# Optimization experiments

Measured on AMD Instinct MI355X. Metric: run time of the kernel, lower is better.

## Reference

```python
import jax, jax.numpy as jnp
import numpy as np

D_MODEL = 1024
N_HEADS = 16
D_K = D_MODEL // N_HEADS
B, S = 2, 2048
NEG = -1000000000.0


def setup_inputs() -> dict:
    key = jax.random.key(0)
    ks = jax.random.split(key, 11)
    scale = 1.0 / np.sqrt(D_MODEL)
    inp = {
        'q': jax.random.normal(ks[0], (B, S, D_MODEL), jnp.float32),
        'k': jax.random.normal(ks[1], (B, S, D_MODEL), jnp.float32),
        'v': jax.random.normal(ks[2], (B, S, D_MODEL), jnp.float32),
        'mask': jnp.tril(jnp.ones((S, S), dtype=bool))[None, None],  # causal [1,1,S,S]
        'w_q': jax.random.normal(ks[3], (D_MODEL, D_MODEL), jnp.float32) * scale,
        'b_q': jax.random.normal(ks[4], (D_MODEL,), jnp.float32) * 0.01,
        'w_k': jax.random.normal(ks[5], (D_MODEL, D_MODEL), jnp.float32) * scale,
        'b_k': jax.random.normal(ks[6], (D_MODEL,), jnp.float32) * 0.01,
        'w_v': jax.random.normal(ks[7], (D_MODEL, D_MODEL), jnp.float32) * scale,
        'b_v': jax.random.normal(ks[8], (D_MODEL,), jnp.float32) * 0.01,
        'w_o': jax.random.normal(ks[9], (D_MODEL, D_MODEL), jnp.float32) * scale,
        'b_o': jax.random.normal(ks[10], (D_MODEL,), jnp.float32) * 0.01,
    }
    return inp


def _split_heads(x):
    b, s, _ = x.shape
    return x.reshape(b, s, N_HEADS, D_K).transpose(0, 2, 1, 3)  # [b,h,s,dk]


def reference(q, k, v, mask, w_q, b_q, w_k, b_k, w_v, b_v, w_o, b_o):
    # Linear projections (torch Linear: x @ W.T + b)
    qh = _split_heads(q @ w_q.T + b_q)
    kh = _split_heads(k @ w_k.T + b_k)
    vh = _split_heads(v @ w_v.T + b_v)
    # scaled dot-product attention (dropout is identity in eval)
    scores = jnp.einsum('bhqd,bhkd->bhqk', qh, kh) / jnp.sqrt(jnp.float32(D_K))
    scores = jnp.where(mask, scores, NEG)
    attn_weights = jax.nn.softmax(scores, axis=-1)
    out = jnp.einsum('bhqk,bhkd->bhqd', attn_weights, vh)
    out = out.transpose(0, 2, 1, 3).reshape(q.shape[0], -1, D_MODEL)
    out = out @ w_o.T + b_o
    return out, attn_weights
```

## Files before the change

kernel.cpp:

```cpp
#include <hip/hip_runtime.h>
#include <hip/hip_bf16.h>


#define DM 1024
#define NH 16
#define DKH 64
#define BB 2
#define SS 2048
#define MM (BB*SS)

typedef __bf16 bf16_t;
typedef __bf16 bf16x4 __attribute__((ext_vector_type(4)));
typedef __bf16 bf16x8 __attribute__((ext_vector_type(8)));
typedef float  f32x4  __attribute__((ext_vector_type(4)));

#define EXP2F(x) __builtin_amdgcn_exp2f(x)

__device__ __forceinline__ f32x4 mfma16(bf16x8 a, bf16x8 b, f32x4 c) {
    return __builtin_amdgcn_mfma_f32_16x16x32_bf16(a, b, c, 0, 0, 0);
}
__device__ __forceinline__ bf16x8 cat8(bf16x4 lo, bf16x4 hi) {
    bf16x8 r;
    r[0]=lo[0]; r[1]=lo[1]; r[2]=lo[2]; r[3]=lo[3];
    r[4]=hi[0]; r[5]=hi[1]; r[6]=hi[2]; r[7]=hi[3];
    return r;
}

__device__ __forceinline__ void gload16(const bf16_t* g, bf16_t* l) {
    __builtin_amdgcn_global_load_lds(
        (const __attribute__((address_space(1))) void*)g,
        (__attribute__((address_space(3))) void*)l, 16, 0, 0);
}

__device__ __forceinline__ bf16x8 ldsw(const bf16_t* t, int row, int ch) {
    return *(const bf16x8*)(t + row * 64 + (((ch ^ row) & 7) << 3));
}

__global__ __launch_bounds__(256)
void cvt_bf16(const float* __restrict__ s0, const float* __restrict__ s1,
              const float* __restrict__ s2, const float* __restrict__ s3,
              bf16_t* __restrict__ d0, bf16_t* __restrict__ d1,
              bf16_t* __restrict__ d2, bf16_t* __restrict__ d3)
{
    const float* ss[4] = {s0, s1, s2, s3};
    bf16_t*      dd[4] = {d0, d1, d2, d3};
    const float* s = ss[blockIdx.y];
    bf16_t*      d = dd[blockIdx.y];
    size_t i = (size_t)(blockIdx.x * 256 + threadIdx.x) * 8;
    float4 f0 = *(const float4*)(s + i);
    float4 f1 = *(const float4*)(s + i + 4);
    bf16x8 v;
    v[0]=(bf16_t)f0.x; v[1]=(bf16_t)f0.y; v[2]=(bf16_t)f0.z; v[3]=(bf16_t)f0.w;
    v[4]=(bf16_t)f1.x; v[5]=(bf16_t)f1.y; v[6]=(bf16_t)f1.z; v[7]=(bf16_t)f1.w;
    *(bf16x8*)(d + i) = v;
}

template<int MODE>
__global__ __launch_bounds__(256)
void mha_gemm5(const bf16_t* __restrict__ A, const bf16_t* __restrict__ W,
               const float* __restrict__ bias, void* __restrict__ out)
{
    __shared__ bf16_t As[2][128 * 64];
    __shared__ bf16_t Bs[2][64 * 64];

    const int tid  = threadIdx.x;
    const int lane = tid & 63;
    const int wid  = tid >> 6;
    const int wm = wid >> 1, wn = wid & 1;
    const int bid  = blockIdx.x;
    const int xcd  = bid & 7, slot = bid >> 3;
    const int bm   = xcd * 4 + (slot >> 4);
    const int bn   = slot & 15;
    const int c = lane & 15, g = lane >> 4;
    const int sr = tid >> 3, sch = tid & 7;
    const int scol = ((sch ^ (sr & 7)) << 3);

    f32x4 acc[4][2] = {};

    const bf16_t* Ab = A + (size_t)(bm * 128 + sr) * DM + scol;
    const bf16_t* Wb = W + (size_t)(bn * 64 + sr) * DM + scol;

#define GSTAGE(buf, kt)  do {                                              \
        bf16_t* asl = &As[buf][wid * 512];                                 \
        bf16_t* bsl = &Bs[buf][wid * 512];                                 \
        _Pragma("unroll")                                                  \
        for (int j = 0; j < 4; ++j)                                        \
            gload16(Ab + (size_t)(j * 32) * DM + (kt) * 64, asl + j * 2048);\
        _Pragma("unroll")                                                  \
        for (int j = 0; j < 2; ++j)                                        \
            gload16(Wb + (size_t)(j * 32) * DM + (kt) * 64, bsl + j * 2048);\
    } while (0)

    GSTAGE(0, 0);
    for (int kt = 0; kt < DM / 64; ++kt) {
        const int cur = kt & 1;
        __syncthreads();
        if (kt + 1 < DM / 64) GSTAGE(cur ^ 1, kt + 1);
        const bf16_t* as = As[cur];
        const bf16_t* bs = Bs[cur];
        #pragma unroll
        for (int kh = 0; kh < 2; ++kh) {
            bf16x8 am[4], bw[2];
            #pragma unroll
            for (int f = 0; f < 4; ++f)
                am[f] = ldsw(as, wm * 64 + f * 16 + c, kh * 4 + g);
            #pragma unroll
            for (int f = 0; f < 2; ++f)
                bw[f] = ldsw(bs, wn * 32 + f * 16 + c, kh * 4 + g);
            #pragma unroll
            for (int fm = 0; fm < 4; ++fm)
                #pragma unroll
                for (int fn = 0; fn < 2; ++fn)
                    acc[fm][fn] = mfma16(am[fm], bw[fn], acc[fm][fn]);
        }
    }
#undef GSTAGE

    #pragma unroll
    for (int fm = 0; fm < 4; ++fm) {
        #pragma unroll
        for (int fn = 0; fn < 2; ++fn) {
            const int col = bn * 64 + wn * 32 + fn * 16 + c;
            const float bcol = bias[col];
            if constexpr (MODE == 2) {
                const int h = (col >> 6) & 15, dk = col & 63;
                const int row0 = bm * 128 + wm * 64 + fm * 16 + 4 * g;
                const int b = row0 >> 11, s0 = row0 & (SS - 1);
                bf16x4 pv;
                #pragma unroll
                for (int r = 0; r < 4; ++r) pv[r] = (bf16_t)(acc[fm][fn][r] + bcol);
                size_t idx = ((size_t)((b * NH + h) * DKH + dk)) * SS
                           + ((s0 >> 5) << 5) + g * 8 + (fm & 1) * 4;
                *(bf16x4*)&((bf16_t*)out)[idx] = pv;
            } else {
                #pragma unroll
                for (int r = 0; r < 4; ++r) {
                    const int row = bm * 128 + wm * 64 + fm * 16 + 4 * g + r;
                    float val = acc[fm][fn][r] + bcol;
                    if constexpr (MODE == 3) {
                        __builtin_nontemporal_store(
                            val, &((float*)out)[(size_t)row * DM + col]);
                    } else {
                        if constexpr (MODE == 0)
                            val *= 0.125f * 1.44269504f;
                        const int b = row >> 11, s = row & (SS - 1);
                        const int h = (col >> 6) & 15;
                        const int fnl = (col >> 4) & 3;
                        const int pos = ((fnl >> 1) << 5) + ((c >> 2) << 3)
                                      + ((fnl & 1) << 2) + (c & 3);
                        ((bf16_t*)out)[((size_t)(b * NH + h) * SS + s) * DKH + pos]
                            = (bf16_t)val;
                    }
                }
            }
        }
    }
}

__global__ __launch_bounds__(256)
void mha_attn12(const bf16_t* __restrict__ Qp, const bf16_t* __restrict__ Kp,
                const bf16_t* __restrict__ Vt, float* __restrict__ attn,
                bf16_t* __restrict__ aout)
{
    __shared__ bf16_t Ks[2][8192];
    __shared__ bf16_t Vs[2][8192];

    const int tid = threadIdx.x, lane = tid & 63, w = tid >> 6;
    const int c = lane & 15, g = lane >> 4;
    const int jb = blockIdx.x, bh = blockIdx.y;
    const int b = bh >> 4, h = bh & 15;

    const int qtA = jb, qtB = 31 - jb;
    const int q0A = qtA * 64, q0B = qtB * 64;
    const int q0wA = q0A + w * 16, q0wB = q0B + w * 16;
    const int ntA = qtA + 1, ntB = qtB + 1;
    const int nr = (ntB + 1) >> 1;

    const bf16_t* Qb = Qp + (size_t)bh * SS * DKH;
    const bf16_t* Kb = Kp + (size_t)bh * SS * DKH;
    const bf16_t* Vb = Vt + (size_t)bh * DKH * SS;
    float* attb = attn + (size_t)bh * SS * SS;

    const int sr = tid >> 3, sch = tid & 7;
    const int ssw = ((sch ^ (sr & 7)) << 3);

    const bf16_t* qrA = Qb + (size_t)(q0wA + c) * DKH;
    const bf16x8 qaA0 = *(const bf16x8*)(qrA + g * 8);
    const bf16x8 qaA1 = *(const bf16x8*)(qrA + 32 + g * 8);
    const bf16_t* qrB = Qb + (size_t)(q0wB + c) * DKH;
    const bf16x8 qaB0 = *(const bf16x8*)(qrB + g * 8);
    const bf16x8 qaB1 = *(const bf16x8*)(qrB + 32 + g * 8);

#define STAGE_K(buf, rr) do {                                               \
        const bf16_t* s0_ = Kb + (size_t)(2 * (rr)) * 4096 + sr * 64 + ssw; \
        gload16(s0_,        &Ks[buf][w * 512]);                             \
        gload16(s0_ + 2048, &Ks[buf][2048 + w * 512]);                      \
        gload16(s0_ + 4096, &Ks[buf][4096 + w * 512]);                      \
        gload16(s0_ + 6144, &Ks[buf][6144 + w * 512]);                      \
    } while (0)

#define STAGE_V(buf, rr) do {                                               \
        const bf16_t* v0_ = Vb + (size_t)sr * SS + (2 * (rr)) * 64 + ssw;   \
        gload16(v0_,                        &Vs[buf][w * 512]);             \
        gload16(v0_ + (size_t)32 * SS,      &Vs[buf][2048 + w * 512]);      \
        gload16(v0_ + 64,                   &Vs[buf][4096 + w * 512]);      \
        gload16(v0_ + (size_t)32 * SS + 64, &Vs[buf][6144 + w * 512]);      \
    } while (0)

    STAGE_K(0, 0);
    float lsumA = 0.f, lsumB = 0.f;
    for (int rr = 0; rr < nr; ++rr) {
        const int cur = rr & 1;
        __syncthreads();
        if (rr + 1 < nr) STAGE_K(cur ^ 1, rr + 1);
        #pragma unroll
        for (int t = 0; t < 2; ++t) {
            const int kt = 2 * rr + t;
            if (kt < ntB) {
                const bf16_t* ks = &Ks[cur][t * 4096];
                {
                    f32x4 s[4] = {};
                    #pragma unroll
                    for (int sb = 0; sb < 4; ++sb) {
                        bf16x8 k0 = ldsw(ks, sb * 16 + c, g);
                        bf16x8 k1 = ldsw(ks, sb * 16 + c, 4 | g);
                        s[sb] = mfma16(k0, qaB0, s[sb]);
                        s[sb] = mfma16(k1, qaB1, s[sb]);
                    }
                    if (kt == qtB) {
                        #pragma unroll
                        for (int sb = 0; sb < 4; ++sb)
                            #pragma unroll
                            for (int r = 0; r < 4; ++r)
                                if (sb * 16 + 4 * g + r <= w * 16 + c)
                                    lsumB += EXP2F(s[sb][r]);
                    } else {
                        #pragma unroll
                        for (int sb = 0; sb < 4; ++sb)
                            #pragma unroll
                            for (int r = 0; r < 4; ++r)
                                lsumB += EXP2F(s[sb][r]);
                    }
                }
                if (kt < ntA) {
                    f32x4 s[4] = {};
                    #pragma unroll
                    for (int sb = 0; sb < 4; ++sb) {
                        bf16x8 k0 = ldsw(ks, sb * 16 + c, g);
                        bf16x8 k1 = ldsw(ks, sb * 16 + c, 4 | g);
                        s[sb] = mfma16(k0, qaA0, s[sb]);
                        s[sb] = mfma16(k1, qaA1, s[sb]);
                    }
                    if (kt == qtA) {
                        #pragma unroll
                        for (int sb = 0; sb < 4; ++sb)
                            #pragma unroll
                            for (int r = 0; r < 4; ++r)
                                if (sb * 16 + 4 * g + r <= w * 16 + c)
                                    lsumA += EXP2F(s[sb][r]);
                    } else {
                        #pragma unroll
                        for (int sb = 0; sb < 4; ++sb)
                            #pragma unroll
                            for (int r = 0; r < 4; ++r)
                                lsumA += EXP2F(s[sb][r]);
                    }
                }
            }
        }
    }
    lsumA += __shfl_xor(lsumA, 16);
    lsumA += __shfl_xor(lsumA, 32);
    lsumB += __shfl_xor(lsumB, 16);
    lsumB += __shfl_xor(lsumB, 32);
    const float invlA = 1.f / lsumA;
    const float invlB = 1.f / lsumB;

    __syncthreads();
    STAGE_K(0, 0);
    STAGE_V(0, 0);
    f32x4 oA[4] = {}, oB[4] = {};
    for (int rr = 0; rr < nr; ++rr) {
        const int cur = rr & 1;
        __syncthreads();
        if (rr + 1 < nr) {
            STAGE_K(cur ^ 1, rr + 1);
            STAGE_V(cur ^ 1, rr + 1);
        }
        #pragma unroll
        for (int t = 0; t < 2; ++t) {
            const int kt = 2 * rr + t;
            if (kt < ntB) {
                const bf16_t* ks = &Ks[cur][t * 4096];
                const bf16_t* vs = &Vs[cur][t * 4096];
                {
                    f32x4 s[4] = {};
                    #pragma unroll
                    for (int sb = 0; sb < 4; ++sb) {
                        bf16x8 k0 = ldsw(ks, sb * 16 + c, g);
                        bf16x8 k1 = ldsw(ks, sb * 16 + c, 4 | g);
                        s[sb] = mfma16(k0, qaB0, s[sb]);
                        s[sb] = mfma16(k1, qaB1, s[sb]);
                    }
                    const bool diag = (kt == qtB);
                    bf16x4 pb[4];
                    float* prow = attb + (size_t)(q0wB + c) * SS + kt * 64 + 4 * g;
                    #pragma unroll
                    for (int sb = 0; sb < 4; ++sb) {
                        f32x4 pf;
                        #pragma unroll
                        for (int r = 0; r < 4; ++r) {
                            bool msk = diag && (sb * 16 + 4 * g + r > w * 16 + c);
                            float p = msk ? 0.f : EXP2F(s[sb][r]) * invlB;
                            pf[r] = p;
                            pb[sb][r] = (bf16_t)p;
                        }
                        *(f32x4*)(prow + sb * 16) = pf;
                    }
                    const bf16x8 pa0 = cat8(pb[0], pb[1]);
                    const bf16x8 pa1 = cat8(pb[2], pb[3]);
                    #pragma unroll
                    for (int fn = 0; fn < 4; ++fn) {
                        bf16x8 v0 = ldsw(vs, fn * 16 + c, g);
                        bf16x8 v1 = ldsw(vs, fn * 16 + c, 4 | g);
                        oB[fn] = mfma16(pa0, v0, oB[fn]);
                        oB[fn] = mfma16(pa1, v1, oB[fn]);
                    }
                }
                if (kt < ntA) {
                    f32x4 s[4] = {};
                    #pragma unroll
                    for (int sb = 0; sb < 4; ++sb) {
                        bf16x8 k0 = ldsw(ks, sb * 16 + c, g);
                        bf16x8 k1 = ldsw(ks, sb * 16 + c, 4 | g);
                        s[sb] = mfma16(k0, qaA0, s[sb]);
                        s[sb] = mfma16(k1, qaA1, s[sb]);
                    }
                    const bool diag = (kt == qtA);
                    bf16x4 pb[4];
                    float* prow = attb + (size_t)(q0wA + c) * SS + kt * 64 + 4 * g;
                    #pragma unroll
                    for (int sb = 0; sb < 4; ++sb) {
                        f32x4 pf;
                        #pragma unroll
                        for (int r = 0; r < 4; ++r) {
                            bool msk = diag && (sb * 16 + 4 * g + r > w * 16 + c);
                            float p = msk ? 0.f : EXP2F(s[sb][r]) * invlA;
                            pf[r] = p;
                            pb[sb][r] = (bf16_t)p;
                        }
                        *(f32x4*)(prow + sb * 16) = pf;
                    }
                    const bf16x8 pa0 = cat8(pb[0], pb[1]);
                    const bf16x8 pa1 = cat8(pb[2], pb[3]);
                    #pragma unroll
                    for (int fn = 0; fn < 4; ++fn) {
                        bf16x8 v0 = ldsw(vs, fn * 16 + c, g);
                        bf16x8 v1 = ldsw(vs, fn * 16 + c, 4 | g);
                        oA[fn] = mfma16(pa0, v0, oA[fn]);
                        oA[fn] = mfma16(pa1, v1, oA[fn]);
                    }
                }
            }
        }
    }
#undef STAGE_K
#undef STAGE_V

    #pragma unroll
    for (int fn = 0; fn < 4; ++fn)
        #pragma unroll
        for (int r = 0; r < 4; ++r) {
            aout[(size_t)(b * SS + q0wB + 4 * g + r) * DM + h * DKH + fn * 16 + c]
                = (bf16_t)oB[fn][r];
            aout[(size_t)(b * SS + q0wA + 4 * g + r) * DM + h * DKH + fn * 16 + c]
                = (bf16_t)oA[fn][r];
        }

    {
        f32x4 z = {0.f, 0.f, 0.f, 0.f};
        {
            const int zr = q0A + (tid >> 2);
            float* dst = attb + (size_t)zr * SS;
            for (int col = ntA * 64 + (tid & 3) * 4; col < SS; col += 16)
                *(f32x4*)(dst + col) = z;
        }
        {
            const int zr = q0B + (tid >> 2);
            float* dst = attb + (size_t)zr * SS;
            for (int col = ntB * 64 + (tid & 3) * 4; col < SS; col += 16)
                *(f32x4*)(dst + col) = z;
        }
    }
}

extern "C" void kernel_launch(void* const* d_in, const int* in_sizes, int n_in,
                              void* d_out, int out_size, void* d_ws, size_t ws_size,
                              hipStream_t stream)
{
    const float* q   = (const float*)d_in[0];
    const float* k   = (const float*)d_in[1];
    const float* v   = (const float*)d_in[2];
    const float* w_q = (const float*)d_in[4];
    const float* b_q = (const float*)d_in[5];
    const float* w_k = (const float*)d_in[6];
    const float* b_k = (const float*)d_in[7];
    const float* w_v = (const float*)d_in[8];
    const float* b_v = (const float*)d_in[9];
    const float* w_o = (const float*)d_in[10];
    const float* b_o = (const float*)d_in[11];

    float* out   = (float*)d_out;
    float* attnw = out + (size_t)MM * DM;

    bf16_t* Qp   = (bf16_t*)d_ws;
    bf16_t* Kp   = Qp + (size_t)MM * DM;
    bf16_t* Vt   = Kp + (size_t)MM * DM;
    bf16_t* aout = Vt + (size_t)MM * DM;
    bf16_t* qb   = aout + (size_t)MM * DM;
    bf16_t* kb   = qb + (size_t)MM * DM;
    bf16_t* vb   = kb + (size_t)MM * DM;
    bf16_t* wqb  = vb + (size_t)MM * DM;
    bf16_t* wkb  = wqb + (size_t)DM * DM;
    bf16_t* wvb  = wkb + (size_t)DM * DM;
    bf16_t* wob  = wvb + (size_t)DM * DM;

    cvt_bf16<<<dim3(MM * DM / 2048, 3), 256, 0, stream>>>(q, k, v, q, qb, kb, vb, qb);
    cvt_bf16<<<dim3(DM * DM / 2048, 4), 256, 0, stream>>>(w_q, w_k, w_v, w_o,
                                                          wqb, wkb, wvb, wob);

    mha_gemm5<0><<<512, 256, 0, stream>>>(qb, wqb, b_q, Qp);
    mha_gemm5<1><<<512, 256, 0, stream>>>(kb, wkb, b_k, Kp);
    mha_gemm5<2><<<512, 256, 0, stream>>>(vb, wvb, b_v, Vt);

    mha_attn12<<<dim3(16, BB * NH), 256, 0, stream>>>(Qp, Kp, Vt, attnw, aout);

    mha_gemm5<3><<<512, 256, 0, stream>>>(aout, wob, b_o, out);
}
```

Before: 247.0 us.

## Merge conversion and QKV launches, stage four K tiles in first attention pass

```diff
diff --git a/kernel.cpp b/kernel.cpp
--- a/kernel.cpp
+++ b/kernel.cpp
@@ -37,28 +37,41 @@
 }
 
 __global__ __launch_bounds__(256)
-void cvt_bf16(const float* __restrict__ s0, const float* __restrict__ s1,
-              const float* __restrict__ s2, const float* __restrict__ s3,
-              bf16_t* __restrict__ d0, bf16_t* __restrict__ d1,
-              bf16_t* __restrict__ d2, bf16_t* __restrict__ d3)
-{
-    const float* ss[4] = {s0, s1, s2, s3};
-    bf16_t*      dd[4] = {d0, d1, d2, d3};
-    const float* s = ss[blockIdx.y];
-    bf16_t*      d = dd[blockIdx.y];
-    size_t i = (size_t)(blockIdx.x * 256 + threadIdx.x) * 8;
+void cvt_all(const float* __restrict__ q, const float* __restrict__ k,
+             const float* __restrict__ v, const float* __restrict__ wq,
+             const float* __restrict__ wk, const float* __restrict__ wv,
+             const float* __restrict__ wo,
+             bf16_t* __restrict__ qb, bf16_t* __restrict__ kb,
+             bf16_t* __restrict__ vb, bf16_t* __restrict__ wqb,
+             bf16_t* __restrict__ wkb, bf16_t* __restrict__ wvb,
+             bf16_t* __restrict__ wob)
+{
+    const int y = blockIdx.y;
+    const float* s;
+    bf16_t* d;
+    size_t i;
+    if (y < 3) {
+        s = (y == 0) ? q : (y == 1) ? k : v;
+        d = (y == 0) ? qb : (y == 1) ? kb : vb;
+        i = (size_t)(blockIdx.x * 256 + threadIdx.x) * 8;
+    } else {
+        const int t = blockIdx.x >> 9;
+        s = (t == 0) ? wq : (t == 1) ? wk : (t == 2) ? wv : wo;
+        d = (t == 0) ? wqb : (t == 1) ? wkb : (t == 2) ? wvb : wob;
+        i = (size_t)((blockIdx.x & 511) * 256 + threadIdx.x) * 8;
+    }
     float4 f0 = *(const float4*)(s + i);
     float4 f1 = *(const float4*)(s + i + 4);
-    bf16x8 v;
-    v[0]=(bf16_t)f0.x; v[1]=(bf16_t)f0.y; v[2]=(bf16_t)f0.z; v[3]=(bf16_t)f0.w;
-    v[4]=(bf16_t)f1.x; v[5]=(bf16_t)f1.y; v[6]=(bf16_t)f1.z; v[7]=(bf16_t)f1.w;
-    *(bf16x8*)(d + i) = v;
-}
-
-template<int MODE>
-__global__ __launch_bounds__(256)
-void mha_gemm5(const bf16_t* __restrict__ A, const bf16_t* __restrict__ W,
-               const float* __restrict__ bias, void* __restrict__ out)
+    bf16x8 o;
+    o[0]=(bf16_t)f0.x; o[1]=(bf16_t)f0.y; o[2]=(bf16_t)f0.z; o[3]=(bf16_t)f0.w;
+    o[4]=(bf16_t)f1.x; o[5]=(bf16_t)f1.y; o[6]=(bf16_t)f1.z; o[7]=(bf16_t)f1.w;
+    *(bf16x8*)(d + i) = o;
+}
+
+__device__ __forceinline__
+void gemm_core(const bf16_t* __restrict__ A, const bf16_t* __restrict__ W,
+               const float* __restrict__ bias, void* __restrict__ out,
+               int bid, int mode)
 {
     __shared__ bf16_t As[2][128 * 64];
     __shared__ bf16_t Bs[2][64 * 64];
@@ -67,7 +80,6 @@
     const int lane = tid & 63;
     const int wid  = tid >> 6;
     const int wm = wid >> 1, wn = wid & 1;
-    const int bid  = blockIdx.x;
     const int xcd  = bid & 7, slot = bid >> 3;
     const int bm   = xcd * 4 + (slot >> 4);
     const int bn   = slot & 15;
@@ -122,7 +134,7 @@
         for (int fn = 0; fn < 2; ++fn) {
             const int col = bn * 64 + wn * 32 + fn * 16 + c;
             const float bcol = bias[col];
-            if constexpr (MODE == 2) {
+            if (mode == 2) {
                 const int h = (col >> 6) & 15, dk = col & 63;
                 const int row0 = bm * 128 + wm * 64 + fm * 16 + 4 * g;
                 const int b = row0 >> 11, s0 = row0 & (SS - 1);
@@ -137,11 +149,11 @@
                 for (int r = 0; r < 4; ++r) {
                     const int row = bm * 128 + wm * 64 + fm * 16 + 4 * g + r;
                     float val = acc[fm][fn][r] + bcol;
-                    if constexpr (MODE == 3) {
+                    if (mode == 3) {
                         __builtin_nontemporal_store(
                             val, &((float*)out)[(size_t)row * DM + col]);
                     } else {
-                        if constexpr (MODE == 0)
+                        if (mode == 0)
                             val *= 0.125f * 1.44269504f;
                         const int b = row >> 11, s = row & (SS - 1);
                         const int h = (col >> 6) & 15;
@@ -158,12 +170,37 @@
 }
 
 __global__ __launch_bounds__(256)
-void mha_attn12(const bf16_t* __restrict__ Qp, const bf16_t* __restrict__ Kp,
+void mha_gemm_qkv(const bf16_t* __restrict__ qb, const bf16_t* __restrict__ kb,
+                  const bf16_t* __restrict__ vb,
+                  const bf16_t* __restrict__ wqb, const bf16_t* __restrict__ wkb,
+                  const bf16_t* __restrict__ wvb,
+                  const float* __restrict__ b_q, const float* __restrict__ b_k,
+                  const float* __restrict__ b_v,
+                  bf16_t* __restrict__ Qp, bf16_t* __restrict__ Kp,
+                  bf16_t* __restrict__ Vt)
+{
+    const int proj = blockIdx.x >> 9;
+    const int bid  = blockIdx.x & 511;
+    const bf16_t* A = (proj == 0) ? qb : (proj == 1) ? kb : vb;
+    const bf16_t* W = (proj == 0) ? wqb : (proj == 1) ? wkb : wvb;
+    const float* bi = (proj == 0) ? b_q : (proj == 1) ? b_k : b_v;
+    void* out       = (proj == 0) ? (void*)Qp : (proj == 1) ? (void*)Kp : (void*)Vt;
+    gemm_core(A, W, bi, out, bid, proj);
+}
+
+__global__ __launch_bounds__(256)
+void mha_gemm_o(const bf16_t* __restrict__ aout, const bf16_t* __restrict__ wob,
+                const float* __restrict__ b_o, float* __restrict__ out)
+{
+    gemm_core(aout, wob, b_o, out, blockIdx.x, 3);
+}
+
+__global__ __launch_bounds__(256)
+void mha_attn13(const bf16_t* __restrict__ Qp, const bf16_t* __restrict__ Kp,
                 const bf16_t* __restrict__ Vt, float* __restrict__ attn,
                 bf16_t* __restrict__ aout)
 {
-    __shared__ bf16_t Ks[2][8192];
-    __shared__ bf16_t Vs[2][8192];
+    __shared__ bf16_t SB[32768];
 
     const int tid = threadIdx.x, lane = tid & 63, w = tid >> 6;
     const int c = lane & 15, g = lane >> 4;
@@ -174,7 +211,6 @@
     const int q0A = qtA * 64, q0B = qtB * 64;
     const int q0wA = q0A + w * 16, q0wB = q0B + w * 16;
     const int ntA = qtA + 1, ntB = qtB + 1;
-    const int nr = (ntB + 1) >> 1;
 
     const bf16_t* Qb = Qp + (size_t)bh * SS * DKH;
     const bf16_t* Kb = Kp + (size_t)bh * SS * DKH;
@@ -191,33 +227,32 @@
     const bf16x8 qaB0 = *(const bf16x8*)(qrB + g * 8);
     const bf16x8 qaB1 = *(const bf16x8*)(qrB + 32 + g * 8);
 
-#define STAGE_K(buf, rr) do {                                               \
-        const bf16_t* s0_ = Kb + (size_t)(2 * (rr)) * 4096 + sr * 64 + ssw; \
-        gload16(s0_,        &Ks[buf][w * 512]);                             \
-        gload16(s0_ + 2048, &Ks[buf][2048 + w * 512]);                      \
-        gload16(s0_ + 4096, &Ks[buf][4096 + w * 512]);                      \
-        gload16(s0_ + 6144, &Ks[buf][6144 + w * 512]);                      \
+#define STAGE_K4(dst, rr) do {                                              \
+        const bf16_t* s0_ = Kb + (size_t)(4 * (rr)) * 4096 + sr * 64 + ssw; \
+        bf16_t* d_ = (dst);                                                 \
+        gload16(s0_,         d_ + w * 512);                                 \
+        gload16(s0_ + 2048,  d_ + 2048 + w * 512);                          \
+        gload16(s0_ + 4096,  d_ + 4096 + w * 512);                          \
+        gload16(s0_ + 6144,  d_ + 6144 + w * 512);                          \
+        gload16(s0_ + 8192,  d_ + 8192 + w * 512);                          \
+        gload16(s0_ + 10240, d_ + 10240 + w * 512);                         \
+        gload16(s0_ + 12288, d_ + 12288 + w * 512);                         \
+        gload16(s0_ + 14336, d_ + 14336 + w * 512);                         \
     } while (0)
 
-#define STAGE_V(buf, rr) do {                                               \
-        const bf16_t* v0_ = Vb + (size_t)sr * SS + (2 * (rr)) * 64 + ssw;   \
-        gload16(v0_,                        &Vs[buf][w * 512]);             \
-        gload16(v0_ + (size_t)32 * SS,      &Vs[buf][2048 + w * 512]);      \
-        gload16(v0_ + 64,                   &Vs[buf][4096 + w * 512]);      \
-        gload16(v0_ + (size_t)32 * SS + 64, &Vs[buf][6144 + w * 512]);      \
-    } while (0)
-
-    STAGE_K(0, 0);
+    const int nr4 = (ntB + 3) >> 2;
+    STAGE_K4(SB, 0);
     float lsumA = 0.f, lsumB = 0.f;
-    for (int rr = 0; rr < nr; ++rr) {
+    for (int rr = 0; rr < nr4; ++rr) {
         const int cur = rr & 1;
         __syncthreads();
-        if (rr + 1 < nr) STAGE_K(cur ^ 1, rr + 1);
+        if (rr + 1 < nr4) STAGE_K4((cur ^ 1) ? SB + 16384 : SB, rr + 1);
+        const bf16_t* kbase = cur ? SB + 16384 : SB;
         #pragma unroll
-        for (int t = 0; t < 2; ++t) {
-            const int kt = 2 * rr + t;
+        for (int t = 0; t < 4; ++t) {
+            const int kt = 4 * rr + t;
             if (kt < ntB) {
-                const bf16_t* ks = &Ks[cur][t * 4096];
+                const bf16_t* ks = kbase + t * 4096;
                 {
                     f32x4 s[4] = {};
                     #pragma unroll
@@ -269,6 +304,7 @@
             }
         }
     }
+#undef STAGE_K4
     lsumA += __shfl_xor(lsumA, 16);
     lsumA += __shfl_xor(lsumA, 32);
     lsumB += __shfl_xor(lsumB, 16);
@@ -276,23 +312,44 @@
     const float invlA = 1.f / lsumA;
     const float invlB = 1.f / lsumB;
 
+#define STAGE_K2(dst, rr) do {                                              \
+        const bf16_t* s0_ = Kb + (size_t)(2 * (rr)) * 4096 + sr * 64 + ssw; \
+        bf16_t* d_ = (dst);                                                 \
+        gload16(s0_,        d_ + w * 512);                                  \
+        gload16(s0_ + 2048, d_ + 2048 + w * 512);                           \
+        gload16(s0_ + 4096, d_ + 4096 + w * 512);                           \
+        gload16(s0_ + 6144, d_ + 6144 + w * 512);                           \
+    } while (0)
+
+#define STAGE_V2(dst, rr) do {                                              \
+        const bf16_t* v0_ = Vb + (size_t)sr * SS + (2 * (rr)) * 64 + ssw;   \
+        bf16_t* d_ = (dst);                                                 \
+        gload16(v0_,                        d_ + w * 512);                  \
+        gload16(v0_ + (size_t)32 * SS,      d_ + 2048 + w * 512);           \
+        gload16(v0_ + 64,                   d_ + 4096 + w * 512);           \
+        gload16(v0_ + (size_t)32 * SS + 64, d_ + 6144 + w * 512);           \
+    } while (0)
+
+    const int nr2 = (ntB + 1) >> 1;
     __syncthreads();
-    STAGE_K(0, 0);
-    STAGE_V(0, 0);
+    STAGE_K2(SB, 0);
+    STAGE_V2(SB + 16384, 0);
     f32x4 oA[4] = {}, oB[4] = {};
-    for (int rr = 0; rr < nr; ++rr) {
+    for (int rr = 0; rr < nr2; ++rr) {
         const int cur = rr & 1;
         __syncthreads();
-        if (rr + 1 < nr) {
-            STAGE_K(cur ^ 1, rr + 1);
-            STAGE_V(cur ^ 1, rr + 1);
-        }
+        if (rr + 1 < nr2) {
+            STAGE_K2((cur ^ 1) ? SB + 8192 : SB, rr + 1);
+            STAGE_V2((cur ^ 1) ? SB + 24576 : SB + 16384, rr + 1);
+        }
+        const bf16_t* kbase = cur ? SB + 8192 : SB;
+        const bf16_t* vbase = cur ? SB + 24576 : SB + 16384;
         #pragma unroll
         for (int t = 0; t < 2; ++t) {
             const int kt = 2 * rr + t;
             if (kt < ntB) {
-                const bf16_t* ks = &Ks[cur][t * 4096];
-                const bf16_t* vs = &Vs[cur][t * 4096];
+                const bf16_t* ks = kbase + t * 4096;
+                const bf16_t* vs = vbase + t * 4096;
                 {
                     f32x4 s[4] = {};
                     #pragma unroll
@@ -364,8 +421,8 @@
             }
         }
     }
-#undef STAGE_K
-#undef STAGE_V
+#undef STAGE_K2
+#undef STAGE_V2
 
     #pragma unroll
     for (int fn = 0; fn < 4; ++fn)
@@ -425,15 +482,13 @@
     bf16_t* wvb  = wkb + (size_t)DM * DM;
     bf16_t* wob  = wvb + (size_t)DM * DM;
 
-    cvt_bf16<<<dim3(MM * DM / 2048, 3), 256, 0, stream>>>(q, k, v, q, qb, kb, vb, qb);
-    cvt_bf16<<<dim3(DM * DM / 2048, 4), 256, 0, stream>>>(w_q, w_k, w_v, w_o,
-                                                          wqb, wkb, wvb, wob);
-
-    mha_gemm5<0><<<512, 256, 0, stream>>>(qb, wqb, b_q, Qp);
-    mha_gemm5<1><<<512, 256, 0, stream>>>(kb, wkb, b_k, Kp);
-    mha_gemm5<2><<<512, 256, 0, stream>>>(vb, wvb, b_v, Vt);
-
-    mha_attn12<<<dim3(16, BB * NH), 256, 0, stream>>>(Qp, Kp, Vt, attnw, aout);
-
-    mha_gemm5<3><<<512, 256, 0, stream>>>(aout, wob, b_o, out);
-}
+    cvt_all<<<dim3(2048, 4), 256, 0, stream>>>(q, k, v, w_q, w_k, w_v, w_o,
+                                               qb, kb, vb, wqb, wkb, wvb, wob);
+
+    mha_gemm_qkv<<<1536, 256, 0, stream>>>(qb, kb, vb, wqb, wkb, wvb,
+                                           b_q, b_k, b_v, Qp, Kp, Vt);
+
+    mha_attn13<<<dim3(16, BB * NH), 256, 0, stream>>>(Qp, Kp, Vt, attnw, aout);
+
+    mha_gemm_o<<<512, 256, 0, stream>>>(aout, wob, b_o, out);
+}
```

New measurement: 230.3 us. 1.07x faster.
